# Kernel optimization log

Hardware: AMD Instinct MI355X
Metric: run time of the kernel (lower is better)

The kernel has to match this reference:

```python
import jax, jax.numpy as jnp
import numpy as np

THETA = 10.0      # spike threshold
TAU_SR = 10.0     # synaptic (psp) alpha-kernel time constant
TAU_REF = 1.0     # refractory alpha-kernel time constant
SCALE_REF = 2.0   # refractory kernel scale (refKernel = -2*theta*alpha)
TS = 1.0          # simulation step


def psp(x):
    """SLAYER psp: causal conv along time with alpha kernel k[n] = (n*Ts/tau)*exp(1 - n*Ts/tau),
    realized exactly as a 2-state linear IIR recurrence. x: (..., T)."""
    a = jnp.float32(np.exp(-TS / TAU_SR))
    c = jnp.float32(np.e * TS / TAU_SR)
    xt = jnp.moveaxis(x, -1, 0)  # (T, ...)
    z = jnp.zeros_like(xt[0])

    def step(carry, xin):
        p, q = carry
        q = a * q + a * p          # q[n] = sum_m x[m]*(n-m)*a^(n-m)
        p = a * p + xin            # p[n] = sum_m x[m]*a^(n-m)
        return (p, q), c * q       # k-convolution output (k[0] = 0)

    _, y = jax.lax.scan(step, (z, z), xt)
    return jnp.moveaxis(y, 0, -1)


def spike(x):
    """SLAYER spike: threshold with refractory feedback. At each step the membrane is
    psp input plus -2*theta * (alpha-kernel conv of past spikes); spike amplitude 1/Ts = 1.
    Refractory alpha kernel realized with the same 2-state IIR. x: (..., T)."""
    a = jnp.float32(np.exp(-TS / TAU_REF))
    c = jnp.float32(np.e * TS / TAU_REF)
    xt = jnp.moveaxis(x, -1, 0)
    z = jnp.zeros_like(xt[0])

    def step(carry, ut):
        p, q = carry
        q = a * q + a * p
        u = ut - SCALE_REF * THETA * c * q   # membrane = input psp + refractory response
        s = (u >= THETA).astype(ut.dtype)
        p = a * p + s                        # spike feeds refractory state (k[0]=0 so no self-effect)
        return (p, q), s

    _, y = jax.lax.scan(step, (z, z), xt)
    return jnp.moveaxis(y, 0, -1)


def conv_t(x, w, pad):
    """Per-timestep 2D conv: x (B,Cin,H,W,T), w (Cout,Cin,k,k); time folded into batch."""
    b, cin, h, wd, t = x.shape
    xt = jnp.moveaxis(x, -1, 1).reshape(b * t, cin, h, wd)
    y = jax.lax.conv_general_dilated(xt, w, (1, 1), [(pad, pad), (pad, pad)])
    y = y.reshape(b, t, y.shape[1], y.shape[2], y.shape[3])
    return jnp.moveaxis(y, 1, -1)


def pool2(x):
    """SLAYER pool: zero-pad odd dims, 2x2 sum with constant weight 1.1*theta, stride 2."""
    b, ch, h, wd, t = x.shape
    ph, pw = (-h) % 2, (-wd) % 2
    x = jnp.pad(x, ((0, 0), (0, 0), (0, ph), (0, pw), (0, 0)))
    h2, w2 = (h + ph) // 2, (wd + pw) // 2
    x = x.reshape(b, ch, h2, 2, w2, 2, t).sum(axis=(3, 5))
    return 1.1 * THETA * x


def setup_inputs() -> dict:
    key = jax.random.key(0)
    ks = jax.random.split(key, 6)
    B, T = 4, 300
    s_in = (jax.random.uniform(ks[0], (B, 2, 34, 34, T)) < 0.03).astype(jnp.float32)
    def w(k, shape, scale):
        fan_in = int(np.prod(shape[1:]))
        return jax.random.normal(k, shape, jnp.float32) * (scale / np.sqrt(fan_in))
    return {
        "s_in": s_in,
        "Wc1": w(ks[1], (24, 2, 5, 5), 10.0),    # weightScale=10
        "Wc2": w(ks[2], (48, 24, 3, 3), 15.0),   # weightScale=15
        "Wc3": w(ks[3], (96, 48, 3, 3), 15.0),   # weightScale=15
        "Wd4a": w(ks[4], (256, 96, 5, 5), 1.0),
        "Wd4b": w(ks[5], (10, 256), 1.0),
    }


def reference(s_in, Wc1, Wc2, Wc3, Wd4a, Wd4b):
    x = spike(psp(conv_t(s_in, Wc1, 2)))                  # (B,24,34,34,T)
    x = spike(psp(pool2(x)))                              # (B,24,17,17,T)
    x = spike(psp(conv_t(x, Wc2, 1)))                     # (B,48,17,17,T)
    x = spike(psp(pool2(x)))                              # (B,48,9,9,T)
    x = spike(psp(conv_t(x, Wc3, 1)))                     # (B,96,9,9,T)
    x = spike(psp(pool2(x)))                              # (B,96,5,5,T)
    x = spike(psp(jnp.einsum('bchwt,ochw->bot', x, Wd4a)))  # (B,256,T)
    x = spike(psp(jnp.einsum('bnt,on->bot', x, Wd4b)))      # (B,10,T)
    return x
```

## Files before the change

kernel.cpp:

```cpp
#include <hip/hip_runtime.h>


#define TT 300

#define A1 0.9048374180359595f
#define C1 0.2718281828459045f
#define A2 0.36787944117144233f
#define C2 2.718281828459045f
#define KREF (20.0f * C2)
#define THETA_F 10.0f

typedef float v2f __attribute__((ext_vector_type(2)));
typedef float f32x4 __attribute__((ext_vector_type(4)));
typedef short bf16x8 __attribute__((ext_vector_type(8)));

struct IIR {
  float p1, q1, p2, q2;
  __device__ IIR() : p1(0.f), q1(0.f), p2(0.f), q2(0.f) {}
  __device__ inline float step(float xin) {
    q1 = A1 * q1 + A1 * p1;
    float y = C1 * q1;
    p1 = A1 * p1 + xin;
    q2 = A2 * q2 + A2 * p2;
    float u = y - KREF * q2;
    float s = (u >= THETA_F) ? 1.0f : 0.0f;
    p2 = A2 * p2 + s;
    return s;
  }
};

__global__ __launch_bounds__(256) void transpose_rc(const float* __restrict__ in,
                                                    float* __restrict__ out,
                                                    int R, int C) {
  __shared__ float tile[64][65];
  int c0 = blockIdx.x * 64, r0 = blockIdx.y * 64;
  int tx = threadIdx.x & 63, ty = threadIdx.x >> 6;
  for (int i = ty; i < 64; i += 4) {
    int r = r0 + i, c = c0 + tx;
    if (r < R && c < C) tile[i][tx] = in[(long)r * C + c];
  }
  __syncthreads();
  for (int i = ty; i < 64; i += 4) {
    int c = c0 + i, r = r0 + tx;
    if (c < C && r < R) out[(long)c * R + r] = tile[tx][i];
  }
}

__device__ inline unsigned rne_bf16_bits(float f) {
  unsigned u = __float_as_uint(f);
  return (u + 0x7FFFu + ((u >> 16) & 1u)) >> 16;
}
template <int CIN, int KS, int CO, int MT, int KC, int CL>
__global__ __launch_bounds__(256) void prep_mfma(const float* __restrict__ Wc,
                                                 ushort* __restrict__ Wm) {
  constexpr int K = CIN * KS * KS;
  constexpr int PLANE = MT * KC * 512;
  int i = blockIdx.x * 256 + threadIdx.x;
  if (i >= PLANE) return;
  int e = i & 7, l = (i >> 3) & 63;
  int rest = i >> 9;
  int kc = rest % KC, m = rest / KC;
  int co = m * 16 + (l & 15);
  int k = kc * 32 + (l >> 4) * 8 + e;
  float w = 0.f;
  if (k < K && co < CO) {
    int ci, dy, dx;
    if (CL) {
      ci = k % CIN;
      int r = k / CIN;
      dy = r / KS;
      dx = r % KS;
    } else {
      ci = k / (KS * KS);
      int r = k % (KS * KS);
      dy = r / KS;
      dx = r % KS;
    }
    w = Wc[((co * CIN + ci) * KS + dy) * KS + dx];
  }
  unsigned b0 = rne_bf16_bits(w);
  float f0 = __uint_as_float(b0 << 16);
  float d1 = w - f0;
  unsigned b1 = rne_bf16_bits(d1);
  float f1 = __uint_as_float(b1 << 16);
  unsigned b2 = rne_bf16_bits(d1 - f1);
  Wm[i] = (ushort)b0;
  Wm[PLANE + i] = (ushort)b1;
  Wm[2 * PLANE + i] = (ushort)b2;
}

template <int CIN, int HW, int KS, int PAD, int CO, int RS, int NW, int NSUB>
__global__ __launch_bounds__(NW * 64) void conv_mfma_d(const float* __restrict__ S,
                                                       const ushort* __restrict__ Wm,
                                                       float* __restrict__ U) {
  constexpr int PH = HW + 2 * PAD;
  constexpr int K = CIN * KS * KS;
  constexpr int KC = (K + 31) / 32;
  constexpr int MT = (CO + 15) / 16;
  constexpr int N = HW * HW;
  constexpr int NT = (N + 15) / 16;
  constexpr int NG = (NT + NSUB - 1) / NSUB;
  constexpr int TILE = CIN * PH * RS;
  constexpr int KPAD = KC * 32;
  __shared__ float lin[TILE];
  __shared__ int koff[KPAD];
  const int t = blockIdx.x, b = blockIdx.y, B = gridDim.y;
  const int tid = threadIdx.x;

  for (int i = tid; i < TILE; i += NW * 64) lin[i] = 0.f;
  for (int k = tid; k < KPAD; k += NW * 64) {
    int ci = k / (KS * KS), r = k % (KS * KS), dy = r / KS, dx = r % KS;
    koff[k] = (k < K) ? (ci * PH * RS + dy * RS + dx) : 0;
  }
  __syncthreads();
  const float* src = S + ((long)t * B + b) * (CIN * N);
  for (int i = tid; i < CIN * N; i += NW * 64) {
    int ci = i / N, r = i % N, iy = r / HW, ix = r % HW;
    lin[ci * PH * RS + (iy + PAD) * RS + ix + PAD] = src[i];
  }
  __syncthreads();

  const int lane = tid & 63;
  const int wv = tid >> 6;
  const int g = lane >> 4;
  const int col = lane & 15;

  bf16x8 af[3 * MT * KC];
#pragma unroll
  for (int f = 0; f < 3 * MT * KC; ++f)
    af[f] = *(const bf16x8*)(Wm + (long)f * 512 + lane * 8);

  for (int grp = wv; grp < NG; grp += NW) {
    const int px0 = grp * (16 * NSUB);
    bool vs[NSUB];
    int pxb[NSUB];
    bf16x8 bf[NSUB][KC];
#pragma unroll
    for (int s = 0; s < NSUB; ++s) {
      int px = px0 + s * 16 + col;
      vs[s] = px < N;
      int ppx = vs[s] ? px : 0;
      int y = ppx / HW, x = ppx % HW;
      pxb[s] = y * RS + x;
#pragma unroll
      for (int kc = 0; kc < KC; ++kc) {
        bf16x8 v;
#pragma unroll
        for (int e = 0; e < 8; ++e) {
          float val = lin[pxb[s] + koff[kc * 32 + g * 8 + e]];
          v[e] = (short)(__float_as_uint(val) >> 16);
        }
        bf[s][kc] = v;
      }
    }

#pragma unroll
    for (int m = 0; m < MT; ++m) {
      f32x4 acc[NSUB];
#pragma unroll
      for (int s = 0; s < NSUB; ++s) acc[s] = (f32x4){0.f, 0.f, 0.f, 0.f};
#pragma unroll
      for (int p = 0; p < 3; ++p) {
#pragma unroll
        for (int kc = 0; kc < KC; ++kc) {
          bf16x8 a = af[(p * MT + m) * KC + kc];
#pragma unroll
          for (int s = 0; s < NSUB; ++s)
            acc[s] = __builtin_amdgcn_mfma_f32_16x16x32_bf16(a, bf[s][kc], acc[s], 0, 0, 0);
        }
      }
      const int co0 = m * 16 + g * 4;
#pragma unroll
      for (int s = 0; s < NSUB; ++s) {
        if (vs[s]) {
          float* up = U + (((long)t * B + b) * CO + co0) * N + px0 + s * 16 + col;
#pragma unroll
          for (int j = 0; j < 4; ++j)
            if (co0 + j < CO) up[(long)j * N] = acc[s][j];
        }
      }
    }
  }
}

template <int CIN, int HW, int KS, int PAD, int CO, int CPAD, int NW, int MCHUNK>
__global__ __launch_bounds__(NW * 64) void conv_mfma_v(const float* __restrict__ S,
                                                       const ushort* __restrict__ Wm,
                                                       float* __restrict__ U) {
  constexpr int PW = HW + 2 * PAD;
  constexpr int K = CIN * KS * KS;
  constexpr int KC = (K + 31) / 32;
  constexpr int KPAD = KC * 32;
  constexpr int RMAX = (KPAD - 1) / CIN;
  constexpr int DYMAX = RMAX / KS;
  constexpr int PHA = (HW + DYMAX > PW) ? (HW + DYMAX) : PW;
  constexpr int MT = CO / 16;
  constexpr int N = HW * HW;
  constexpr int NT = (N + 15) / 16;
  constexpr int NCH = MT / MCHUNK;
  constexpr int CROWS = MCHUNK * 16;
  __shared__ ushort linb[PHA * PW * CPAD];
  __shared__ int offb[KC * 4];
  __shared__ float cst[CROWS * N];
  const int t = blockIdx.x, b = blockIdx.y, B = gridDim.y;
  const int tid = threadIdx.x;

  for (int i = tid; i < PHA * PW * CPAD / 2; i += NW * 64) ((int*)linb)[i] = 0;
  for (int i = tid; i < KC * 4; i += NW * 64) {
    int k0 = (i >> 2) * 32 + (i & 3) * 8;
    int ci0 = k0 % CIN, r0 = k0 / CIN;
    offb[i] = ((r0 / KS) * PW + (r0 % KS)) * CPAD + ci0;
  }
  __syncthreads();
  const float* src = S + ((long)t * B + b) * (CIN * N);
  for (int i = tid; i < CIN * N; i += NW * 64) {
    int ci = i / N, r = i % N, iy = r / HW, ix = r % HW;
    linb[((iy + PAD) * PW + ix + PAD) * CPAD + ci] =
        (ushort)(__float_as_uint(src[i]) >> 16);
  }
  __syncthreads();

  const int lane = tid & 63;
  const int wv = tid >> 6;
  const int g = lane >> 4;
  const int col = lane & 15;

  int boff[KC];
#pragma unroll
  for (int kc = 0; kc < KC; ++kc) boff[kc] = offb[kc * 4 + g];

  for (int ch = blockIdx.z; ch < NCH; ch += gridDim.z) {
    for (int nt = wv; nt < NT; nt += NW) {
      int px = nt * 16 + col;
      bool vpx = px < N;
      int ppx = vpx ? px : 0;
      int y = ppx / HW, x = ppx % HW;
      const int pxb = (y * PW + x) * CPAD;

      bf16x8 bf[KC];
#pragma unroll
      for (int kc = 0; kc < KC; ++kc)
        bf[kc] = *(const bf16x8*)(linb + pxb + boff[kc]);

#pragma unroll
      for (int ml = 0; ml < MCHUNK; ++ml) {
        const int m = ch * MCHUNK + ml;
        f32x4 acc = {0.f, 0.f, 0.f, 0.f};
#pragma unroll
        for (int p = 0; p < 3; ++p) {
#pragma unroll
          for (int kc = 0; kc < KC; ++kc) {
            bf16x8 a = *(const bf16x8*)(Wm + ((long)(p * MT + m) * KC + kc) * 512 + lane * 8);
            acc = __builtin_amdgcn_mfma_f32_16x16x32_bf16(a, bf[kc], acc, 0, 0, 0);
          }
        }
        if (vpx) {
          const int r0 = ml * 16 + g * 4;
#pragma unroll
          for (int j = 0; j < 4; ++j) cst[(r0 + j) * N + px] = acc[j];
        }
      }
    }
    __syncthreads();
    const f32x4* cs = (const f32x4*)cst;
    f32x4* ug = (f32x4*)(U + (((long)t * B + b) * CO + ch * CROWS) * N);
    for (int i = tid; i < CROWS * N / 4; i += NW * 64) ug[i] = cs[i];
    __syncthreads();
  }
}

template <int CIN, int HW, int KS, int PAD, int CO, int CPAD, int NW>
__global__ __launch_bounds__(NW * 64) void conv_mfma_w(const float* __restrict__ S,
                                                       const ushort* __restrict__ Wm,
                                                       float* __restrict__ U) {
  constexpr int PW = HW + 2 * PAD;
  constexpr int K = CIN * KS * KS;
  constexpr int KC = (K + 31) / 32;
  constexpr int KPAD = KC * 32;
  constexpr int RMAX = (KPAD - 1) / CIN;
  constexpr int DYMAX = RMAX / KS;
  constexpr int PHA = (HW + DYMAX > PW) ? (HW + DYMAX) : PW;
  constexpr int MT = CO / 16;
  static_assert(MT == NW, "wave per m-tile");
  constexpr int N = HW * HW;
  constexpr int NT = (N + 15) / 16;
  constexpr int KCB = 7;
  constexpr int KB = KC / KCB;
  static_assert(KC % KCB == 0, "KCB divides KC");
  __shared__ ushort linb[PHA * PW * CPAD];
  __shared__ int offb[KC * 4];
  __shared__ float cst[CO * N];
  const int t = blockIdx.x, b = blockIdx.y, B = gridDim.y;
  const int tid = threadIdx.x;

  for (int i = tid; i < PHA * PW * CPAD / 2; i += NW * 64) ((int*)linb)[i] = 0;
  for (int i = tid; i < KC * 4; i += NW * 64) {
    int k0 = (i >> 2) * 32 + (i & 3) * 8;
    int ci0 = k0 % CIN, r0 = k0 / CIN;
    offb[i] = ((r0 / KS) * PW + (r0 % KS)) * CPAD + ci0;
  }
  __syncthreads();
  const float* src = S + ((long)t * B + b) * (CIN * N);
  for (int i = tid; i < CIN * N; i += NW * 64) {
    int ci = i / N, r = i % N, iy = r / HW, ix = r % HW;
    linb[((iy + PAD) * PW + ix + PAD) * CPAD + ci] =
        (ushort)(__float_as_uint(src[i]) >> 16);
  }
  __syncthreads();

  const int lane = tid & 63;
  const int m = tid >> 6;
  const int g = lane >> 4;
  const int col = lane & 15;

  int boff[KC];
#pragma unroll
  for (int kc = 0; kc < KC; ++kc) boff[kc] = offb[kc * 4 + g];

  int pxb[NT];
#pragma unroll
  for (int nt = 0; nt < NT; ++nt) {
    int px = nt * 16 + col;
    int ppx = (px < N) ? px : 0;
    int y = ppx / HW, x = ppx % HW;
    pxb[nt] = (y * PW + x) * CPAD;
  }

  f32x4 acc[NT];
#pragma unroll
  for (int nt = 0; nt < NT; ++nt) acc[nt] = (f32x4){0.f, 0.f, 0.f, 0.f};

  for (int p = 0; p < 3; ++p) {
#pragma unroll 1
    for (int kb = 0; kb < KB; ++kb) {
      bf16x8 af[KCB];
#pragma unroll
      for (int q = 0; q < KCB; ++q)
        af[q] = *(const bf16x8*)(Wm + ((long)(p * MT + m) * KC + kb * KCB + q) * 512 + lane * 8);
#pragma unroll 1
      for (int nt = 0; nt < NT; ++nt) {
#pragma unroll
        for (int q = 0; q < KCB; ++q) {
          bf16x8 bf = *(const bf16x8*)(linb + pxb[nt] + boff[kb * KCB + q]);
          acc[nt] = __builtin_amdgcn_mfma_f32_16x16x32_bf16(af[q], bf, acc[nt], 0, 0, 0);
        }
      }
    }
  }

  const int r0 = m * 16 + g * 4;
#pragma unroll
  for (int nt = 0; nt < NT; ++nt) {
    int px = nt * 16 + col;
    if (px < N) {
#pragma unroll
      for (int j = 0; j < 4; ++j) cst[(r0 + j) * N + px] = acc[nt][j];
    }
  }
  __syncthreads();
  const f32x4* cs = (const f32x4*)cst;
  f32x4* ug = (f32x4*)(U + (((long)t * B + b) * CO) * N);
  for (int i = tid; i < CO * N / 4; i += NW * 64) ug[i] = cs[i];
}

template <int C, int HIN, int HOUT>
__global__ __launch_bounds__(128) void ppp4_tm(const float* __restrict__ U,
                                               float* __restrict__ out, int B) {
  const int NOUT = B * C * HOUT * HOUT;
  const long SIN = (long)B * C * HIN * HIN;
  int id = blockIdx.x * 128 + threadIdx.x;
  int sub = id & 3, m = id >> 2;
  bool active = m < NOUT;
  int mm = active ? m : 0;
  int x2 = mm % HOUT;
  int y2 = (mm / HOUT) % HOUT;
  int c = (mm / (HOUT * HOUT)) % C;
  int b = mm / (C * HOUT * HOUT);
  int iy = 2 * y2 + (sub >> 1), ix = 2 * x2 + (sub & 1);
  bool valid = active && iy < HIN && ix < HIN;
  const float* base = U + ((long)(b * C + c) * HIN + iy) * HIN + ix;
  bool writer = active && (sub == 0);
  float* op = out + mm;
  IIR si, so;
  float pr0 = valid ? base[0] : 0.f;
  float pr1 = valid ? base[SIN] : 0.f;
  float pr2 = valid ? base[2 * SIN] : 0.f;
  float pr3 = valid ? base[3 * SIN] : 0.f;
  for (int tb = 0; tb < TT; tb += 4) {
    float a0 = pr0, a1 = pr1, a2 = pr2, a3 = pr3;
    const float* nb = base + (long)(tb + 4) * SIN;
    pr0 = valid ? nb[0] : 0.f;
    pr1 = valid ? nb[SIN] : 0.f;
    pr2 = valid ? nb[2 * SIN] : 0.f;
    pr3 = valid ? nb[3 * SIN] : 0.f;
    {
      float s = si.step(a0);
      float v = s + __shfl_xor(s, 1); v += __shfl_xor(v, 2);
      float o = so.step(11.0f * v);
      if (writer) op[(long)tb * NOUT] = o;
    }
    {
      float s = si.step(a1);
      float v = s + __shfl_xor(s, 1); v += __shfl_xor(v, 2);
      float o = so.step(11.0f * v);
      if (writer) op[(long)(tb + 1) * NOUT] = o;
    }
    {
      float s = si.step(a2);
      float v = s + __shfl_xor(s, 1); v += __shfl_xor(v, 2);
      float o = so.step(11.0f * v);
      if (writer) op[(long)(tb + 2) * NOUT] = o;
    }
    {
      float s = si.step(a3);
      float v = s + __shfl_xor(s, 1); v += __shfl_xor(v, 2);
      float o = so.step(11.0f * v);
      if (writer) op[(long)(tb + 3) * NOUT] = o;
    }
  }
}

__global__ __launch_bounds__(256) void dense7k(const float* __restrict__ S,
                                               const float* __restrict__ Wt,
                                               float* __restrict__ P) {
  const int r0 = blockIdx.x * 16 + (threadIdx.x >> 6) * 4;
  const int kz = blockIdx.y;
  const int lane = threadIdx.x & 63;
  const float* s0 = S + (long)r0 * 2400;
  const float* s1 = s0 + 2400;
  const float* s2 = s0 + 4800;
  const float* s3 = s0 + 7200;
  const float* wp = Wt + lane * 4;
  v2f aA[4], aB[4];
#pragma unroll
  for (int o = 0; o < 4; ++o) { aA[o] = (v2f)(0.f); aB[o] = (v2f)(0.f); }
  const int k0 = kz * 300, k1 = k0 + 300;
  for (int k = k0; k < k1; k += 4) {
    float4 a0 = *(const float4*)(s0 + k);
    float4 a1 = *(const float4*)(s1 + k);
    float4 a2 = *(const float4*)(s2 + k);
    float4 a3 = *(const float4*)(s3 + k);
#define DSTEP(KK, AX)                                                        \
    {                                                                        \
      float4 w = *(const float4*)(wp + (long)(k + KK) * 256);                \
      v2f pA, pB;                                                            \
      pA.x = a0.AX; pA.y = a1.AX; pB.x = a2.AX; pB.y = a3.AX;                \
      aA[0] += pA * w.x; aA[1] += pA * w.y; aA[2] += pA * w.z; aA[3] += pA * w.w; \
      aB[0] += pB * w.x; aB[1] += pB * w.y; aB[2] += pB * w.z; aB[3] += pB * w.w; \
    }
    DSTEP(0, x) DSTEP(1, y) DSTEP(2, z) DSTEP(3, w)
#undef DSTEP
  }
  float* p = P + (long)kz * 307200 + (long)r0 * 256 + lane * 4;
#pragma unroll
  for (int o = 0; o < 4; ++o) p[o] = aA[o].x;
#pragma unroll
  for (int o = 0; o < 4; ++o) p[256 + o] = aA[o].y;
#pragma unroll
  for (int o = 0; o < 4; ++o) p[512 + o] = aB[o].x;
#pragma unroll
  for (int o = 0; o < 4; ++o) p[768 + o] = aB[o].y;
}

__global__ __launch_bounds__(256) void reduce8(const float* __restrict__ P,
                                               float* __restrict__ U7) {
  int i = blockIdx.x * 256 + threadIdx.x;
  if (i >= 76800) return;
  const float4* p = (const float4*)P;
  float4 a = p[i];
#pragma unroll
  for (int kz = 1; kz < 8; ++kz) {
    float4 b = p[(long)kz * 76800 + i];
    a.x += b.x; a.y += b.y; a.z += b.z; a.w += b.w;
  }
  ((float4*)U7)[i] = a;
}

__global__ __launch_bounds__(128) void psp7(const float* __restrict__ U7,
                                            float* __restrict__ out) {
  int n = blockIdx.x * 128 + threadIdx.x;
  IIR st;
  float pr0 = U7[n], pr1 = U7[1024 + n], pr2 = U7[2048 + n], pr3 = U7[3072 + n];
  for (int tb = 0; tb < TT; tb += 4) {
    float a0 = pr0, a1 = pr1, a2 = pr2, a3 = pr3;
    const float* nb = U7 + (long)(tb + 4) * 1024 + n;
    pr0 = nb[0]; pr1 = nb[1024]; pr2 = nb[2048]; pr3 = nb[3072];
    out[(long)tb * 1024 + n] = st.step(a0);
    out[(long)(tb + 1) * 1024 + n] = st.step(a1);
    out[(long)(tb + 2) * 1024 + n] = st.step(a2);
    out[(long)(tb + 3) * 1024 + n] = st.step(a3);
  }
}

__global__ __launch_bounds__(256) void dense8(const float* __restrict__ S,
                                              const float* __restrict__ W,
                                              float* __restrict__ U) {
  int id = blockIdx.x * 256 + threadIdx.x;
  if (id >= 12000) return;
  int o = id % 10, row = id / 10;
  const float* sr = S + (long)row * 256;
  const float* wr = W + o * 256;
  float acc = 0.f;
  for (int k = 0; k < 256; k += 4) {
    float4 a = *(const float4*)(sr + k);
    float4 w = *(const float4*)(wr + k);
    acc += a.x * w.x; acc += a.y * w.y; acc += a.z * w.z; acc += a.w * w.w;
  }
  U[id] = acc;
}

__global__ void psp8_out(const float* __restrict__ U, float* __restrict__ out) {
  int n = threadIdx.x;
  bool act = n < 40;
  int nn = act ? n : 0;
  IIR st;
  float pr0 = U[nn], pr1 = U[40 + nn], pr2 = U[80 + nn], pr3 = U[120 + nn];
  for (int tb = 0; tb < TT; tb += 4) {
    float a0 = pr0, a1 = pr1, a2 = pr2, a3 = pr3;
    const float* nb = U + (long)(tb + 4) * 40 + nn;
    pr0 = nb[0]; pr1 = nb[40]; pr2 = nb[80]; pr3 = nb[120];
    float o0 = st.step(a0), o1 = st.step(a1), o2 = st.step(a2), o3 = st.step(a3);
    if (act) {
      out[nn * TT + tb] = o0;
      out[nn * TT + tb + 1] = o1;
      out[nn * TT + tb + 2] = o2;
      out[nn * TT + tb + 3] = o3;
    }
  }
}

extern "C" void kernel_launch(void* const* d_in, const int* in_sizes, int n_in,
                              void* d_out, int out_size, void* d_ws, size_t ws_size,
                              hipStream_t stream) {
  const float* s_in = (const float*)d_in[0];
  const float* Wc1  = (const float*)d_in[1];
  const float* Wc2  = (const float*)d_in[2];
  const float* Wc3  = (const float*)d_in[3];
  const float* Wd4a = (const float*)d_in[4];
  const float* Wd4b = (const float*)d_in[5];

  float* Buf1 = (float*)d_ws;
  float* Buf2 = Buf1 + 33292800;
  float* s2   = Buf2;
  float* s4   = Buf2 + 8323200;
  float* Wt4a = Buf2 + 12988800;
  float* T0   = Buf2 + 13910400;
  float* s7   = Buf2 + 16737840;
  float* P7   = Buf2 + 17045040;
  float* U7   = Buf2 + 19502640;
  float* s6   = Buf2;
  float* U8   = Buf1;
  ushort* Wm1 = (ushort*)P7;
  ushort* Wm2 = Wm1 + 18432;
  ushort* Wm3 = Wm1 + 50688;

  transpose_rc<<<dim3(5, 145), 256, 0, stream>>>(s_in, T0, 9248, 300);
  transpose_rc<<<dim3(38, 4), 256, 0, stream>>>(Wd4a, Wt4a, 256, 2400);
  prep_mfma<2, 5, 24, 2, 2, 0><<<24, 256, 0, stream>>>(Wc1, Wm1);
  prep_mfma<24, 3, 48, 3, 7, 1><<<42, 256, 0, stream>>>(Wc2, Wm2);
  prep_mfma<48, 3, 96, 6, 14, 1><<<168, 256, 0, stream>>>(Wc3, Wm3);

  conv_mfma_d<2, 34, 5, 2, 24, 39, 8, 4><<<dim3(300, 4), 512, 0, stream>>>(T0, Wm1, Buf1);
  ppp4_tm<24, 34, 17><<<867, 128, 0, stream>>>(Buf1, s2, 4);
  conv_mfma_v<24, 17, 3, 1, 48, 24, 8, 1><<<dim3(300, 4), 512, 0, stream>>>(s2, Wm2, Buf1);
  ppp4_tm<48, 17, 9><<<486, 128, 0, stream>>>(Buf1, s4, 4);
  conv_mfma_w<48, 9, 3, 1, 96, 56, 6><<<dim3(300, 4), 384, 0, stream>>>(s4, Wm3, Buf1);
  ppp4_tm<96, 9, 5><<<300, 128, 0, stream>>>(Buf1, s6, 4);
  dense7k<<<dim3(75, 8), 256, 0, stream>>>(s6, Wt4a, P7);
  reduce8<<<300, 256, 0, stream>>>(P7, U7);
  psp7<<<8, 128, 0, stream>>>(U7, s7);
  dense8<<<47, 256, 0, stream>>>(s7, Wd4b, U8);
  psp8_out<<<1, 64, 0, stream>>>(U8, (float*)d_out);
}
```

Baseline: 579.7 us.

## Stage conv weight fragments in LDS and split conv3 output channels across blocks

Conv2's kernel now loads the weight fragments for each 16-channel m-tile into shared memory once per block and reads the A operand from LDS, replacing per-wave global reads. Conv3 is restructured so each wave handles one pixel tile with its B fragments kept in registers. Its weights are staged in LDS per part, and the output channels are split across two z-blocks with three m-tiles each. This is meant to cut redundant global weight traffic and raise parallelism for conv3. The cost is extra LDS use and more barriers, which may lower occupancy.

Measured after the change: 580.1 us. No clear change (+0.1%).

```diff
diff --git a/kernel.cpp b/kernel.cpp
--- a/kernel.cpp
+++ b/kernel.cpp
@@ -183,10 +183,10 @@
   }
 }
 
-template <int CIN, int HW, int KS, int PAD, int CO, int CPAD, int NW, int MCHUNK>
-__global__ __launch_bounds__(NW * 64) void conv_mfma_v(const float* __restrict__ S,
-                                                       const ushort* __restrict__ Wm,
-                                                       float* __restrict__ U) {
+template <int CIN, int HW, int KS, int PAD, int CO, int CPAD, int NW>
+__global__ __launch_bounds__(NW * 64) void conv_mfma_a3(const float* __restrict__ S,
+                                                        const ushort* __restrict__ Wm,
+                                                        float* __restrict__ U) {
   constexpr int PW = HW + 2 * PAD;
   constexpr int K = CIN * KS * KS;
   constexpr int KC = (K + 31) / 32;
@@ -197,11 +197,10 @@
   constexpr int MT = CO / 16;
   constexpr int N = HW * HW;
   constexpr int NT = (N + 15) / 16;
-  constexpr int NCH = MT / MCHUNK;
-  constexpr int CROWS = MCHUNK * 16;
   __shared__ ushort linb[PHA * PW * CPAD];
   __shared__ int offb[KC * 4];
-  __shared__ float cst[CROWS * N];
+  __shared__ uint4 alds4[3 * KC * 64];
+  __shared__ float cst[16 * N];
   const int t = blockIdx.x, b = blockIdx.y, B = gridDim.y;
   const int tid = threadIdx.x;
 
@@ -229,7 +228,13 @@
 #pragma unroll
   for (int kc = 0; kc < KC; ++kc) boff[kc] = offb[kc * 4 + g];
 
-  for (int ch = blockIdx.z; ch < NCH; ch += gridDim.z) {
+  for (int ch = 0; ch < MT; ++ch) {
+    for (int i = tid; i < 3 * KC * 64; i += NW * 64) {
+      int fl = i >> 6, w = i & 63;
+      int p = fl / KC, kc = fl % KC;
+      alds4[i] = ((const uint4*)Wm)[((long)(p * MT + ch) * KC + kc) * 64 + w];
+    }
+    __syncthreads();
     for (int nt = wv; nt < NT; nt += NW) {
       int px = nt * 16 + col;
       bool vpx = px < N;
@@ -242,37 +247,33 @@
       for (int kc = 0; kc < KC; ++kc)
         bf[kc] = *(const bf16x8*)(linb + pxb + boff[kc]);
 
-#pragma unroll
-      for (int ml = 0; ml < MCHUNK; ++ml) {
-        const int m = ch * MCHUNK + ml;
-        f32x4 acc = {0.f, 0.f, 0.f, 0.f};
-#pragma unroll
-        for (int p = 0; p < 3; ++p) {
-#pragma unroll
-          for (int kc = 0; kc < KC; ++kc) {
-            bf16x8 a = *(const bf16x8*)(Wm + ((long)(p * MT + m) * KC + kc) * 512 + lane * 8);
-            acc = __builtin_amdgcn_mfma_f32_16x16x32_bf16(a, bf[kc], acc, 0, 0, 0);
-          }
-        }
-        if (vpx) {
-          const int r0 = ml * 16 + g * 4;
-#pragma unroll
-          for (int j = 0; j < 4; ++j) cst[(r0 + j) * N + px] = acc[j];
+      f32x4 acc = {0.f, 0.f, 0.f, 0.f};
+#pragma unroll
+      for (int p = 0; p < 3; ++p) {
+#pragma unroll
+        for (int kc = 0; kc < KC; ++kc) {
+          bf16x8 a = *(const bf16x8*)((const ushort*)alds4 + (p * KC + kc) * 512 + lane * 8);
+          acc = __builtin_amdgcn_mfma_f32_16x16x32_bf16(a, bf[kc], acc, 0, 0, 0);
         }
       }
+      if (vpx) {
+        const int r0 = g * 4;
+#pragma unroll
+        for (int j = 0; j < 4; ++j) cst[(r0 + j) * N + px] = acc[j];
+      }
     }
     __syncthreads();
     const f32x4* cs = (const f32x4*)cst;
-    f32x4* ug = (f32x4*)(U + (((long)t * B + b) * CO + ch * CROWS) * N);
-    for (int i = tid; i < CROWS * N / 4; i += NW * 64) ug[i] = cs[i];
+    f32x4* ug = (f32x4*)(U + (((long)t * B + b) * CO + ch * 16) * N);
+    for (int i = tid; i < 16 * N / 4; i += NW * 64) ug[i] = cs[i];
     __syncthreads();
   }
 }
 
-template <int CIN, int HW, int KS, int PAD, int CO, int CPAD, int NW>
-__global__ __launch_bounds__(NW * 64) void conv_mfma_w(const float* __restrict__ S,
-                                                       const ushort* __restrict__ Wm,
-                                                       float* __restrict__ U) {
+template <int CIN, int HW, int KS, int PAD, int CO, int CPAD, int NW, int MCHUNK>
+__global__ __launch_bounds__(NW * 64) void conv_mfma_a1(const float* __restrict__ S,
+                                                        const ushort* __restrict__ Wm,
+                                                        float* __restrict__ U) {
   constexpr int PW = HW + 2 * PAD;
   constexpr int K = CIN * KS * KS;
   constexpr int KC = (K + 31) / 32;
@@ -281,16 +282,16 @@
   constexpr int DYMAX = RMAX / KS;
   constexpr int PHA = (HW + DYMAX > PW) ? (HW + DYMAX) : PW;
   constexpr int MT = CO / 16;
-  static_assert(MT == NW, "wave per m-tile");
   constexpr int N = HW * HW;
   constexpr int NT = (N + 15) / 16;
-  constexpr int KCB = 7;
-  constexpr int KB = KC / KCB;
-  static_assert(KC % KCB == 0, "KCB divides KC");
+  static_assert(NT <= NW, "one nt per wave");
+  constexpr int CROWS = MCHUNK * 16;
   __shared__ ushort linb[PHA * PW * CPAD];
   __shared__ int offb[KC * 4];
-  __shared__ float cst[CO * N];
+  __shared__ uint4 alds4[MCHUNK * KC * 64];
+  __shared__ float cst[CROWS * N];
   const int t = blockIdx.x, b = blockIdx.y, B = gridDim.y;
+  const int ch = blockIdx.z;
   const int tid = threadIdx.x;
 
   for (int i = tid; i < PHA * PW * CPAD / 2; i += NW * 64) ((int*)linb)[i] = 0;
@@ -309,58 +310,56 @@
   __syncthreads();
 
   const int lane = tid & 63;
-  const int m = tid >> 6;
+  const int wv = tid >> 6;
   const int g = lane >> 4;
   const int col = lane & 15;
-
-  int boff[KC];
-#pragma unroll
-  for (int kc = 0; kc < KC; ++kc) boff[kc] = offb[kc * 4 + g];
-
-  int pxb[NT];
-#pragma unroll
-  for (int nt = 0; nt < NT; ++nt) {
-    int px = nt * 16 + col;
-    int ppx = (px < N) ? px : 0;
-    int y = ppx / HW, x = ppx % HW;
-    pxb[nt] = (y * PW + x) * CPAD;
-  }
-
-  f32x4 acc[NT];
-#pragma unroll
-  for (int nt = 0; nt < NT; ++nt) acc[nt] = (f32x4){0.f, 0.f, 0.f, 0.f};
+  const bool act = wv < NT;
+  const int nt = act ? wv : 0;
+  const int px = nt * 16 + col;
+  const bool vpx = act && (px < N);
+  const int ppx = vpx ? px : 0;
+  const int y = ppx / HW, x = ppx % HW;
+  const int pxb = (y * PW + x) * CPAD;
+
+  bf16x8 bf[KC];
+#pragma unroll
+  for (int kc = 0; kc < KC; ++kc)
+    bf[kc] = *(const bf16x8*)(linb + pxb + offb[kc * 4 + g]);
+
+  f32x4 acc[MCHUNK];
+#pragma unroll
+  for (int ml = 0; ml < MCHUNK; ++ml) acc[ml] = (f32x4){0.f, 0.f, 0.f, 0.f};
 
   for (int p = 0; p < 3; ++p) {
-#pragma unroll 1
-    for (int kb = 0; kb < KB; ++kb) {
-      bf16x8 af[KCB];
-#pragma unroll
-      for (int q = 0; q < KCB; ++q)
-        af[q] = *(const bf16x8*)(Wm + ((long)(p * MT + m) * KC + kb * KCB + q) * 512 + lane * 8);
-#pragma unroll 1
-      for (int nt = 0; nt < NT; ++nt) {
-#pragma unroll
-        for (int q = 0; q < KCB; ++q) {
-          bf16x8 bf = *(const bf16x8*)(linb + pxb[nt] + boff[kb * KCB + q]);
-          acc[nt] = __builtin_amdgcn_mfma_f32_16x16x32_bf16(af[q], bf, acc[nt], 0, 0, 0);
-        }
+    if (p) __syncthreads();
+    for (int i = tid; i < MCHUNK * KC * 64; i += NW * 64) {
+      int fl = i >> 6, w = i & 63;
+      int ml = fl / KC, kc = fl % KC;
+      alds4[i] = ((const uint4*)Wm)[((long)(p * MT + ch * MCHUNK + ml) * KC + kc) * 64 + w];
+    }
+    __syncthreads();
+#pragma unroll
+    for (int ml = 0; ml < MCHUNK; ++ml) {
+#pragma unroll
+      for (int kc = 0; kc < KC; ++kc) {
+        bf16x8 a = *(const bf16x8*)((const ushort*)alds4 + (ml * KC + kc) * 512 + lane * 8);
+        acc[ml] = __builtin_amdgcn_mfma_f32_16x16x32_bf16(a, bf[kc], acc[ml], 0, 0, 0);
       }
     }
   }
 
-  const int r0 = m * 16 + g * 4;
-#pragma unroll
-  for (int nt = 0; nt < NT; ++nt) {
-    int px = nt * 16 + col;
-    if (px < N) {
-#pragma unroll
-      for (int j = 0; j < 4; ++j) cst[(r0 + j) * N + px] = acc[nt][j];
+  if (vpx) {
+#pragma unroll
+    for (int ml = 0; ml < MCHUNK; ++ml) {
+      const int r0 = ml * 16 + g * 4;
+#pragma unroll
+      for (int j = 0; j < 4; ++j) cst[(r0 + j) * N + px] = acc[ml][j];
     }
   }
   __syncthreads();
   const f32x4* cs = (const f32x4*)cst;
-  f32x4* ug = (f32x4*)(U + (((long)t * B + b) * CO) * N);
-  for (int i = tid; i < CO * N / 4; i += NW * 64) ug[i] = cs[i];
+  f32x4* ug = (f32x4*)(U + (((long)t * B + b) * CO + ch * CROWS) * N);
+  for (int i = tid; i < CROWS * N / 4; i += NW * 64) ug[i] = cs[i];
 }
 
 template <int C, int HIN, int HOUT>
@@ -562,9 +561,9 @@
 
   conv_mfma_d<2, 34, 5, 2, 24, 39, 8, 4><<<dim3(300, 4), 512, 0, stream>>>(T0, Wm1, Buf1);
   ppp4_tm<24, 34, 17><<<867, 128, 0, stream>>>(Buf1, s2, 4);
-  conv_mfma_v<24, 17, 3, 1, 48, 24, 8, 1><<<dim3(300, 4), 512, 0, stream>>>(s2, Wm2, Buf1);
+  conv_mfma_a3<24, 17, 3, 1, 48, 24, 8><<<dim3(300, 4), 512, 0, stream>>>(s2, Wm2, Buf1);
   ppp4_tm<48, 17, 9><<<486, 128, 0, stream>>>(Buf1, s4, 4);
-  conv_mfma_w<48, 9, 3, 1, 96, 56, 6><<<dim3(300, 4), 384, 0, stream>>>(s4, Wm3, Buf1);
+  conv_mfma_a1<48, 9, 3, 1, 96, 56, 6, 3><<<dim3(300, 4, 2), 384, 0, stream>>>(s4, Wm3, Buf1);
   ppp4_tm<96, 9, 5><<<300, 128, 0, stream>>>(Buf1, s6, 4);
   dense7k<<<dim3(75, 8), 256, 0, stream>>>(s6, Wt4a, P7);
   reduce8<<<300, 256, 0, stream>>>(P7, U7);
```
